# Optimization experiments

Hardware: AMD Instinct MI355X
Metric: run time of the kernel (lower is better)

The kernel has to match this reference:

```python
import jax, jax.numpy as jnp
import numpy as np

# edge types: (src_type, dst_type), order fixed to match param stack index
ETYPES = [("tag","question"),("tag","answer"),("tag","comment"),("module","question"),("module","answer"),("question","tag"),("answer","tag"),("comment","tag"),("question","module"),("answer","module")]
NTYPES = ["tag","question","answer","comment","module"]
EKEYS = ["ei_tq","ei_ta","ei_tc","ei_mq","ei_ma","ei_qt","ei_at","ei_ct","ei_qm","ei_am"]
ECOUNT = [500000,1000000,1000000,300000,600000,500000,1000000,1000000,300000,600000]
N = {"tag":5000,"question":50000,"answer":100000,"comment":150000,"module":2000}
H, D, P, G, O = 64, 256, 768, 1024, 2


def setup_inputs() -> dict:
    key = jax.random.key(0)
    ks = iter(jax.random.split(key, 80))
    inp = {}
    for t in NTYPES:
        inp["x_" + t] = jax.random.normal(next(ks), (N[t], D), jnp.float32)
    inp["post_emb"] = jax.random.normal(next(ks), (G, P), jnp.float32)
    for ek, (s, d), E in zip(EKEYS, ETYPES, ECOUNT):
        src = jax.random.randint(next(ks), (E,), 0, N[s])
        dst = jax.random.randint(next(ks), (E,), 0, N[d])
        inp[ek] = jnp.stack([src, dst])
    for t in NTYPES:
        inp["batch_" + t] = jnp.sort(jax.random.randint(next(ks), (N[t],), 0, G))
    for l, din in enumerate([D, H]):
        inp[f"Wsrc{l}"] = 0.05 * jax.random.normal(next(ks), (10, din, H), jnp.float32)
        inp[f"Wdst{l}"] = 0.05 * jax.random.normal(next(ks), (10, din, H), jnp.float32)
        inp[f"asrc{l}"] = 0.05 * jax.random.normal(next(ks), (10, H), jnp.float32)
        inp[f"adst{l}"] = 0.05 * jax.random.normal(next(ks), (10, H), jnp.float32)
        inp[f"b{l}"] = jnp.zeros((10, H), jnp.float32)
    inp["Wlin"] = 0.05 * jax.random.normal(next(ks), (5 * H + P, O), jnp.float32)
    inp["blin"] = jnp.zeros((O,), jnp.float32)
    return inp


def _gat(xs, xd, ei, Ws, Wd, a_s, a_d, b):
    # PyG GATConv (bipartite, heads=1, add_self_loops=False)
    hs = xs @ Ws                      # [Ns, H]
    hd = xd @ Wd                      # [Nd, H]
    src, dst = ei[0], ei[1]
    logits = jax.nn.leaky_relu((hs @ a_s)[src] + (hd @ a_d)[dst], 0.2)  # [E]
    nd = xd.shape[0]
    m = jax.ops.segment_max(logits, dst, num_segments=nd)
    ex = jnp.exp(logits - m[dst])
    den = jax.ops.segment_sum(ex, dst, num_segments=nd)
    alpha = ex / (den[dst] + 1e-16)
    out = jax.ops.segment_sum(hs[src] * alpha[:, None], dst, num_segments=nd)
    return out + b


def _mean_pool(x, batch, num_graphs):
    s = jax.ops.segment_sum(x, batch, num_segments=num_graphs)
    c = jax.ops.segment_sum(jnp.ones((x.shape[0],), x.dtype), batch, num_segments=num_graphs)
    return s / jnp.maximum(c, 1.0)[:, None]


def _forward(xs, eis, layers, batches, post_emb, Wlin, blin):
    x = xs
    for (Ws, Wd, a_s, a_d, b) in layers:
        new = {t: None for t in NTYPES}
        for i, (s, d) in enumerate(ETYPES):
            o = _gat(x[s], x[d], eis[i], Ws[i], Wd[i], a_s[i], a_d[i], b[i])
            new[d] = o if new[d] is None else new[d] + o
        x = {t: jax.nn.relu(v) for t, v in new.items()}
    num_graphs = post_emb.shape[0]
    pooled = [_mean_pool(x[t], batches[t], num_graphs) for t in NTYPES]
    out = jnp.concatenate(pooled + [post_emb], axis=1)   # [G, 5H + P]
    logits = jax.nn.relu(out @ Wlin + blin)
    return jax.nn.softmax(logits, axis=-1)


def reference(x_tag, x_question, x_answer, x_comment, x_module, post_emb,
              ei_tq, ei_ta, ei_tc, ei_mq, ei_ma, ei_qt, ei_at, ei_ct, ei_qm, ei_am,
              batch_tag, batch_question, batch_answer, batch_comment, batch_module,
              Wsrc0, Wdst0, asrc0, adst0, b0, Wsrc1, Wdst1, asrc1, adst1, b1,
              Wlin, blin):
    xs = {"tag": x_tag, "question": x_question, "answer": x_answer, "comment": x_comment, "module": x_module}
    eis = [ei_tq, ei_ta, ei_tc, ei_mq, ei_ma, ei_qt, ei_at, ei_ct, ei_qm, ei_am]
    batches = {"tag": batch_tag, "question": batch_question, "answer": batch_answer, "comment": batch_comment, "module": batch_module}
    layers = [(Wsrc0, Wdst0, asrc0, adst0, b0), (Wsrc1, Wdst1, asrc1, adst1, b1)]
    return _forward(xs, eis, layers, batches, post_emb, Wlin, blin)
```

## Files before the change

### kernel.cpp

```cpp
#include <hip/hip_runtime.h>
#include <math.h>

#define NTY 5
#define NET 10
#define NTOT 307000
#define ETOT 6800000
#define GDIM 1024
#define PDIM 768
#define NGEMMB 7335
#define GSH 2445
#define NBINB 1668
#define NBK 2949
#define NMEGA_C (NBINB + GSH)
#define NMEGA_B (NBINB + GSH)
#define NMEGA_S (NBK + GSH)
#define NPREPB 802

using short8 = __attribute__((ext_vector_type(8))) short;
using f32x4  = __attribute__((ext_vector_type(4))) float;

static const int kSRCT[NET]= {0,0,0,4,4,1,2,3,1,2};
static const int kNT[NTY]  = {5000,50000,100000,150000,2000};
static const int kTOFF[NTY]= {0,5000,55000,155000,305000};
static const int kRB[NET+1]= {0,50000,150000,300000,350000,450000,455000,460000,465000,467000,469000};

__device__ const int gOB[NET]   = {0,50001,150002,300003,350004,450005,455006,460007,465008,467009};
__device__ const int gEB[NET+1] = {0,500000,1500000,2500000,2800000,3400000,3900000,4900000,5900000,6200000,6800000};
__device__ const int gSB[NET]   = {0,5000,10000,15000,17000,19000,69000,169000,319000,369000};
__device__ const int gRB[NET]   = {0,50000,150000,300000,350000,450000,455000,460000,465000,467000};
__device__ const int gND[NET]   = {50000,100000,150000,50000,100000,5000,5000,5000,2000,2000};
__device__ const int gTOFF[NTY] = {0,5000,55000,155000,305000};
__device__ const int gNIN[NTY]  = {3,2,2,1,2};
__device__ const int gINET[NTY][3] = {{5,6,7},{0,3,0},{1,4,0},{2,0,0},{8,9,0}};
__device__ const int gNJ[NET]   = {3,0,0,2,0,2,2,1,0,0};
__device__ const int gTG[NET][3]= {{5,6,7},{0,0,0},{0,0,0},{8,9,0},{0,0,0},{0,3,0},{1,4,0},{2,0,0},{0,0,0},{0,0,0}};
__device__ const int gDSTT[NET] = {1,2,3,1,2,0,0,0,4,4};
__device__ const int gSH[NET]   = {8,8,8,8,8,4,4,4,4,4};
__device__ const int gBKB[NET+1]= {0,196,587,1173,1369,1760,2073,2386,2699,2824,2949};
__device__ const int gBC[NET+1] = {0,123,368,613,687,834,957,1202,1447,1521,1668};

__device__ __forceinline__ unsigned short f2bf(float f){
  unsigned int u = __float_as_uint(f);
  u += 0x7fffu + ((u>>16)&1u);
  return (unsigned short)(u>>16);
}
__device__ __forceinline__ float bf2f(unsigned short h){
  return __uint_as_float(((unsigned int)h)<<16);
}

struct PrepTab {
  const float* Wd0; const float* ad0; const float* b0;
  const float* Wd1; const float* ad1; const float* b1;
  const float* Ws0; const float* Ws1;
  float* wv0; float* wv1; float* bs0; float* bs1;
  unsigned short* Wt0; unsigned short* Wt1;
};
struct PoolTab { const int* batch[NTY]; const float* x[NTY]; int nt[NTY]; };
struct GemmArgs {
  const float* X[NET];
  const unsigned short* Wt;
  const float* asrc;
  const float* wv;
  unsigned short* hs;
  float* ssrc;
  float* sdst;
  int K;
};
struct MCTab {
  GemmArgs g;
  const int* ei[NET];
  int* cntB;
};
struct MBTab {
  GemmArgs g;
  const int* ei[NET];
  int* gcur;
  int2* pairs;
};
struct MSTab {
  GemmArgs g;
  const int2* pairs;
  const int* cntB;
  const int* segB;
  const int* exB;
  int* offs;
  int* csr;
};
struct AggTab {
  const int* offs;
  const int* csr;
  const unsigned short* hs;
  const float* ssrc;
  const float* sdst;
  const float* bsum;
  float* xout;
};

__global__ __launch_bounds__(256) void k_prep(PrepTab p) {
  int b = blockIdx.x;
  int tid = threadIdx.x;
  if (b == 0) {
    for (int e2=0; e2<NET; e2++){
      const float* W = p.Wd0 + (long)e2*256*64;
      const float* a = p.ad0 + e2*64;
      float s=0.f;
      #pragma unroll 8
      for (int c=0;c<64;c++) s += W[tid*64+c]*a[c];
      p.wv0[e2*256+tid]=s;
    }
    for (int idx=tid; idx<320; idx+=256){
      int ty=idx>>6, c=idx&63; float s=0.f;
      #pragma unroll
      for (int i=0;i<NET;i++) if (gDSTT[i]==ty) s += p.b0[i*64+c];
      p.bs0[idx]=s;
    }
    return;
  }
  if (b == 1) {
    if (tid < 64){
      for (int e2=0; e2<NET; e2++){
        const float* W = p.Wd1 + (long)e2*64*64;
        const float* a = p.ad1 + e2*64;
        float s=0.f;
        #pragma unroll 8
        for (int c=0;c<64;c++) s += W[tid*64+c]*a[c];
        p.wv1[e2*256+tid]=s;
      }
    }
    for (int idx=tid; idx<320; idx+=256){
      int ty=idx>>6, c=idx&63; float s=0.f;
      #pragma unroll
      for (int i=0;i<NET;i++) if (gDSTT[i]==ty) s += p.b1[i*64+c];
      p.bs1[idx]=s;
    }
    return;
  }
  if (b < 2+640) {
    int i = b-2;
    int et = i>>6, chunk = i&63;
    int idx = chunk*256 + tid;
    int col = idx>>8, k = idx&255;
    p.Wt0[(long)et*16384 + idx] = f2bf(p.Ws0[(long)et*16384 + k*64 + col]);
    return;
  }
  {
    int i = b-642;
    int et = i>>4, chunk = i&15;
    int idx = chunk*256 + tid;
    int col = idx>>6, k = idx&63;
    p.Wt1[(long)et*4096 + idx] = f2bf(p.Ws1[(long)et*4096 + k*64 + col]);
  }
}

__global__ __launch_bounds__(256) void k_scanB(const int* __restrict__ cntB,
                                               int* __restrict__ segB,
                                               int* __restrict__ gcurB,
                                               int* __restrict__ exB) {
  __shared__ int tp[256], te[256];
  int tid = threadIdx.x;
  int base = tid*12;
  int locP[12], locE[12];
  int sp=0, se=0;
  #pragma unroll
  for (int i=0;i<12;i++){
    int b = base+i;
    int v = (b<NBK) ? cntB[b] : 0;
    locE[i]=se; se += v;
    locP[i]=sp; sp += (v+7)&~7;
  }
  tp[tid]=sp; te[tid]=se; __syncthreads();
  for (int off=1; off<256; off<<=1){
    int xp = (tid>=off)? tp[tid-off] : 0;
    int xe = (tid>=off)? te[tid-off] : 0;
    __syncthreads();
    tp[tid]+=xp; te[tid]+=xe;
    __syncthreads();
  }
  int preP = tp[tid]-sp, preE = te[tid]-se;
  #pragma unroll
  for (int i=0;i<12;i++){
    int b = base+i;
    if (b<NBK){
      int v = preP + locP[i];
      segB[b]=v; gcurB[b]=v;
      exB[b]=preE + locE[i];
    }
  }
}

__device__ __forceinline__ void gemm_block(const GemmArgs& t, int b) {
  __shared__ unsigned short sX[64][72];
  __shared__ unsigned short sWt[64][72];
  __shared__ float sdd[3][64][4];
  const int GB1=79,GB2=158,GB3=237,GB4=269,GB5=301,GB6=1083,GB7=2646,GB8=4990,GB9=5772;
  int et = (b>=GB1)+(b>=GB2)+(b>=GB3)+(b>=GB4)+(b>=GB5)+(b>=GB6)+(b>=GB7)+(b>=GB8)+(b>=GB9);
  const int GBb[NET] = {0,GB1,GB2,GB3,GB4,GB5,GB6,GB7,GB8,GB9};
  const int NSa[NET] = {5000,5000,5000,2000,2000,50000,100000,150000,50000,100000};
  int lb = b - GBb[et];
  int Ns = NSa[et];
  int K = t.K;
  const float* X = t.X[et];
  const unsigned short* Wt = t.Wt + (long)et*64*K;
  const float* avec = t.asrc + et*64;
  int sbase = gSB[et];
  unsigned short* HS = t.hs + (long)sbase*64;
  float* score = t.ssrc + sbase;

  int nj = gNJ[et];
  const float* wvA = t.wv + gTG[et][0]*256;
  const float* wvB = t.wv + gTG[et][1]*256;
  const float* wvC = t.wv + gTG[et][2]*256;

  int tid = threadIdx.x;
  int w = tid>>6, lane = tid&63;
  int row0 = lb*64;
  int l15 = lane&15, lg = lane>>4;
  int arow = w*16 + l15;
  int kgrp = lg*8;
  int drow = tid>>2, dq = tid&3;
  f32x4 acc0={0.f,0.f,0.f,0.f}, acc1={0.f,0.f,0.f,0.f}, acc2={0.f,0.f,0.f,0.f}, acc3={0.f,0.f,0.f,0.f};
  float asd0=0.f, asd1=0.f, asd2=0.f;

  for (int k0=0;k0<K;k0+=64){
    #pragma unroll
    for (int p=0;p<4;p++){
      int r = (tid>>4) + 16*p;
      int c = (tid&15)*4;
      int gr = row0 + r;
      float4 xv = make_float4(0.f,0.f,0.f,0.f);
      if (gr < Ns) xv = *(const float4*)(X + (long)gr*K + k0 + c);
      ushort4 o; o.x=f2bf(xv.x); o.y=f2bf(xv.y); o.z=f2bf(xv.z); o.w=f2bf(xv.w);
      *(ushort4*)&sX[r][c] = o;
    }
    {
      int cq = tid>>2, kq = tid&3;
      const unsigned short* ws = Wt + (long)cq*K + k0;
      #pragma unroll
      for (int it=0; it<4; it++){
        int k = kq*4 + it*16;
        *(ushort4*)&sWt[cq][k] = *(const ushort4*)(ws + k);
      }
    }
    __syncthreads();
    #pragma unroll
    for (int ks=0; ks<64; ks+=32){
      short8 af = *(const short8*)&sX[arow][ks+kgrp];
      short8 b0 = *(const short8*)&sWt[ 0+l15][ks+kgrp];
      short8 b1 = *(const short8*)&sWt[16+l15][ks+kgrp];
      short8 b2 = *(const short8*)&sWt[32+l15][ks+kgrp];
      short8 b3 = *(const short8*)&sWt[48+l15][ks+kgrp];
      acc0 = __builtin_amdgcn_mfma_f32_16x16x32_bf16(af, b0, acc0, 0, 0, 0);
      acc1 = __builtin_amdgcn_mfma_f32_16x16x32_bf16(af, b1, acc1, 0, 0, 0);
      acc2 = __builtin_amdgcn_mfma_f32_16x16x32_bf16(af, b2, acc2, 0, 0, 0);
      acc3 = __builtin_amdgcn_mfma_f32_16x16x32_bf16(af, b3, acc3, 0, 0, 0);
    }
    if (nj) {
      int kb = dq*16;
      #pragma unroll
      for (int kk=0; kk<16; kk++){
        float xv = bf2f(sX[drow][kb+kk]);
        asd0 += xv * wvA[k0+kb+kk];
        asd1 += xv * wvB[k0+kb+kk];
        asd2 += xv * wvC[k0+kb+kk];
      }
    }
    __syncthreads();
  }
  if (nj) {
    sdd[0][drow][dq]=asd0;
    sdd[1][drow][dq]=asd1;
    sdd[2][drow][dq]=asd2;
    __syncthreads();
    if (tid < 64) {
      int r = row0 + tid;
      if (r < Ns) {
        for (int j=0;j<nj;j++) {
          float s = sdd[j][tid][0]+sdd[j][tid][1]+sdd[j][tid][2]+sdd[j][tid][3];
          t.sdst[gRB[gTG[et][j]] + r] = s;
        }
      }
    }
  }
  float av0 = avec[ 0+l15], av1 = avec[16+l15], av2 = avec[32+l15], av3 = avec[48+l15];
  int growb = row0 + w*16 + lg*4;
  #pragma unroll
  for (int r=0;r<4;r++){
    int grow = growb + r;
    if (grow < Ns){
      HS[(long)grow*64 +  0+l15] = f2bf(acc0[r]);
      HS[(long)grow*64 + 16+l15] = f2bf(acc1[r]);
      HS[(long)grow*64 + 32+l15] = f2bf(acc2[r]);
      HS[(long)grow*64 + 48+l15] = f2bf(acc3[r]);
    }
    float s = acc0[r]*av0 + acc1[r]*av1 + acc2[r]*av2 + acc3[r]*av3;
    s += __shfl_xor(s, 1);
    s += __shfl_xor(s, 2);
    s += __shfl_xor(s, 4);
    s += __shfl_xor(s, 8);
    if (l15==0 && grow<Ns) score[grow]=s;
  }
}

__global__ __launch_bounds__(256) void k_gemm_all(GemmArgs t) {
  gemm_block(t, blockIdx.x);
}

__global__ __launch_bounds__(256) void k_megaCount(MCTab t) {
  __shared__ int cnt[640];
  long long b = blockIdx.x;
  const long long G = GSH, T = NMEGA_C;
  long long lo = (b*G)/T, hi = ((b+1)*G)/T;
  if (hi > lo) {
    gemm_block(t.g, (int)lo);
    return;
  }
  int sidx = (int)(b - lo);
  int et=0;
  #pragma unroll
  for (int i=0;i<NET;i++) if (sidx >= gBC[i+1]) et=i+1;
  int lb = sidx - gBC[et];
  int E = gEB[et+1]-gEB[et];
  int e0 = lb*4096;
  int eend = e0+4096; if (eend > E) eend = E;
  int sh = gSH[et];
  int nbk = gBKB[et+1]-gBKB[et];
  const int* D = t.ei[et] + E;
  int tid = threadIdx.x;
  for (int j=tid; j<nbk; j+=256) cnt[j]=0;
  __syncthreads();
  #pragma unroll
  for (int i=0;i<16;i++){
    int idx = e0 + i*256 + tid;
    if (idx < eend) atomicAdd(&cnt[D[idx]>>sh], 1);
  }
  __syncthreads();
  int* cb = t.cntB + gBKB[et];
  for (int j=tid; j<nbk; j+=256) if (cnt[j]) atomicAdd(&cb[j], cnt[j]);
}

__global__ __launch_bounds__(256) void k_megaBin(MBTab t) {
  __shared__ int cnt[640], cnt2[640], gb2[640];
  long long b = blockIdx.x;
  const long long G = GSH, T = NMEGA_B;
  long long lo = (b*G)/T, hi = ((b+1)*G)/T;
  if (hi > lo) {
    gemm_block(t.g, GSH + (int)lo);
    return;
  }
  int sidx = (int)(b - lo);
  int et=0;
  #pragma unroll
  for (int i=0;i<NET;i++) if (sidx >= gBC[i+1]) et=i+1;
  int lb = sidx - gBC[et];
  int E = gEB[et+1]-gEB[et];
  int e0 = lb*4096;
  int eend = e0+4096; if (eend > E) eend = E;
  int sh = gSH[et];
  int nbk = gBKB[et+1]-gBKB[et];
  int bkb = gBKB[et];
  const int* EI = t.ei[et];
  int tid = threadIdx.x;
  int sr[16], dv[16];
  #pragma unroll
  for (int i=0;i<16;i++){
    int idx = e0 + i*256 + tid;
    if (idx < eend){ sr[i]=EI[idx]; dv[i]=EI[E+idx]; } else dv[i] = -1;
  }
  for (int j=tid; j<nbk; j+=256){ cnt[j]=0; cnt2[j]=0; }
  __syncthreads();
  #pragma unroll
  for (int i=0;i<16;i++) if (dv[i]>=0) atomicAdd(&cnt[dv[i]>>sh], 1);
  __syncthreads();
  for (int j=tid; j<nbk; j+=256) if (cnt[j]) gb2[j] = atomicAdd(&t.gcur[bkb+j], cnt[j]);
  __syncthreads();
  #pragma unroll
  for (int i=0;i<16;i++) if (dv[i]>=0){
    int bb = dv[i]>>sh;
    int p = gb2[bb] + atomicAdd(&cnt2[bb], 1);
    t.pairs[p] = make_int2(sr[i], dv[i]);
  }
}

__global__ __launch_bounds__(256) void k_megaScat(MSTab t) {
  __shared__ int cnt[256], sd[256], lcur[256];
  long long b = blockIdx.x;
  const long long G = GSH, T = NMEGA_S;
  long long lo = (b*G)/T, hi = ((b+1)*G)/T;
  if (hi > lo) {
    gemm_block(t.g, 2*GSH + (int)lo);
    return;
  }
  int b2 = (int)(b - lo);
  int et=0;
  #pragma unroll
  for (int i=0;i<NET;i++) if (b2 >= gBKB[i+1]) et=i+1;
  int lb = b2 - gBKB[et];
  int sh = gSH[et];
  int nd = gND[et];
  int d0 = lb<<sh;
  int ndst = (1<<sh); if (d0+ndst > nd) ndst = nd-d0;
  int n = t.cntB[b2];
  const int2* pr = t.pairs + t.segB[b2];
  int csrBase = t.exB[b2] - gEB[et];
  int tid = threadIdx.x;
  cnt[tid]=0;
  __syncthreads();
  for (int i=tid; i<n; i+=256) atomicAdd(&cnt[pr[i].y - d0], 1);
  __syncthreads();
  int v = (tid<ndst)? cnt[tid] : 0;
  sd[tid]=v; __syncthreads();
  for (int off=1; off<256; off<<=1){
    int x = (tid>=off)? sd[tid-off] : 0;
    __syncthreads();
    sd[tid]+=x;
    __syncthreads();
  }
  int excl = sd[tid]-v;
  lcur[tid] = excl;
  if (tid < ndst) t.offs[gOB[et] + d0 + tid] = csrBase + excl;
  if (tid==0 && b2 == gBKB[et+1]-1) t.offs[gOB[et] + nd] = gEB[et+1]-gEB[et];
  __syncthreads();
  int* csrb = t.csr + gEB[et] + csrBase;
  for (int i=tid; i<n; i+=256){
    int2 p = pr[i];
    int pos = atomicAdd(&lcur[p.y - d0], 1);
    csrb[pos] = p.x;
  }
}

__global__ __launch_bounds__(256) void k_agg_all(AggTab t) {
  int nb = blockIdx.x;
  int node0;
  if (nb < 1250)      node0 = nb*4;
  else if (nb < 1750) node0 = 305000 + (nb-1250)*4;
  else                node0 = 5000 + (nb-1750)*4;
  int node = node0 + (threadIdx.x>>6);
  int lane = threadIdx.x & 63;
  int ty = (node>=5000)+(node>=55000)+(node>=155000)+(node>=305000);
  int r = node - gTOFF[ty];
  float outacc = 0.f;
  int ne = gNIN[ty];
  for (int ii=0; ii<ne; ii++) {
    int et = gINET[ty][ii];
    float sd = t.sdst[gRB[et] + r];
    int ob = gOB[et];
    int beg = t.offs[ob + r];
    int end = t.offs[ob + r + 1];
    if (beg >= end) continue;
    const int* cs = t.csr + gEB[et];
    const float* ss = t.ssrc + gSB[et];
    const unsigned short* hsb = t.hs + (long)gSB[et]*64;
    float denl = 0.f, acc = 0.f;
    for (int chunk = beg; chunk < end; chunk += 64) {
      int n = end - chunk; if (n > 64) n = 64;
      int s = 0; float ex = 0.f;
      if (lane < n) {
        s = cs[chunk + lane];
        float l = ss[s] + sd;
        l = (l>0.f)? l : 0.2f*l;
        ex = __expf(l);
      }
      denl += ex;
      unsigned int exu = __float_as_uint(ex);
      int j = 0;
      for (; j+8 <= n; j += 8) {
        int a0=__builtin_amdgcn_readlane(s,j+0), a1=__builtin_amdgcn_readlane(s,j+1);
        int a2=__builtin_amdgcn_readlane(s,j+2), a3=__builtin_amdgcn_readlane(s,j+3);
        int a4=__builtin_amdgcn_readlane(s,j+4), a5=__builtin_amdgcn_readlane(s,j+5);
        int a6=__builtin_amdgcn_readlane(s,j+6), a7=__builtin_amdgcn_readlane(s,j+7);
        float e0=__uint_as_float(__builtin_amdgcn_readlane(exu,j+0));
        float e1=__uint_as_float(__builtin_amdgcn_readlane(exu,j+1));
        float e2=__uint_as_float(__builtin_amdgcn_readlane(exu,j+2));
        float e3=__uint_as_float(__builtin_amdgcn_readlane(exu,j+3));
        float e4=__uint_as_float(__builtin_amdgcn_readlane(exu,j+4));
        float e5=__uint_as_float(__builtin_amdgcn_readlane(exu,j+5));
        float e6=__uint_as_float(__builtin_amdgcn_readlane(exu,j+6));
        float e7=__uint_as_float(__builtin_amdgcn_readlane(exu,j+7));
        float h0=bf2f(hsb[(long)a0*64+lane]);
        float h1=bf2f(hsb[(long)a1*64+lane]);
        float h2=bf2f(hsb[(long)a2*64+lane]);
        float h3=bf2f(hsb[(long)a3*64+lane]);
        float h4=bf2f(hsb[(long)a4*64+lane]);
        float h5=bf2f(hsb[(long)a5*64+lane]);
        float h6=bf2f(hsb[(long)a6*64+lane]);
        float h7=bf2f(hsb[(long)a7*64+lane]);
        acc += e0*h0 + e1*h1 + e2*h2 + e3*h3;
        acc += e4*h4 + e5*h5 + e6*h6 + e7*h7;
      }
      for (; j<n; j++) {
        int aj=__builtin_amdgcn_readlane(s,j);
        float ej=__uint_as_float(__builtin_amdgcn_readlane(exu,j));
        acc += ej * bf2f(hsb[(long)aj*64+lane]);
      }
    }
    #pragma unroll
    for (int off=32; off; off>>=1) denl += __shfl_xor(denl, off);
    outacc += acc/(denl+1e-16f);
  }
  float o = outacc + t.bsum[ty*64+lane];
  t.xout[(long)node*64+lane] = fmaxf(o,0.f);
}

__global__ __launch_bounds__(64) void k_pool(PoolTab t, float* __restrict__ pooled) {
  int g = blockIdx.x; int ty = blockIdx.y; int lane = threadIdx.x;
  const int* batch = t.batch[ty];
  int n = t.nt[ty];
  int lo=0, hi=0;
  if (lane==0){
    int a=0,b2=n;
    while(a<b2){int mm=(a+b2)>>1; if (batch[mm]<g) a=mm+1; else b2=mm;}
    lo=a;
    a=lo; b2=n;
    while(a<b2){int mm=(a+b2)>>1; if (batch[mm]<g+1) a=mm+1; else b2=mm;}
    hi=a;
  }
  lo=__shfl(lo,0); hi=__shfl(hi,0);
  const float* x = t.x[ty];
  float acc=0.f;
  for (int i=lo;i<hi;i++) acc += x[(long)i*64+lane];
  int cnt = hi-lo;
  pooled[(long)g*320 + ty*64 + lane] = acc / (float)(cnt>0?cnt:1);
}

__global__ __launch_bounds__(256) void k_final(
    const float* __restrict__ pooled, const float* __restrict__ post,
    const float* __restrict__ Wlin, const float* __restrict__ blin,
    float* __restrict__ out)
{
  int w = (blockIdx.x*256+threadIdx.x)>>6;
  int lane = threadIdx.x&63;
  if (w>=GDIM) return;
  float a0=0.f,a1=0.f;
  for (int k=lane;k<320+PDIM;k+=64){
    float v = (k<320) ? pooled[(long)w*320+k] : post[(long)w*PDIM + (k-320)];
    a0 += v*Wlin[k*2];
    a1 += v*Wlin[k*2+1];
  }
  #pragma unroll
  for (int off=32;off;off>>=1){ a0+=__shfl_xor(a0,off); a1+=__shfl_xor(a1,off); }
  if (lane==0){
    float z0=a0+blin[0], z1=a1+blin[1];
    z0=fmaxf(z0,0.f); z1=fmaxf(z1,0.f);
    float mm=fmaxf(z0,z1);
    float e0=__expf(z0-mm), e1=__expf(z1-mm);
    float inv = 1.f/(e0+e1);
    out[w*2+0]=e0*inv; out[w*2+1]=e1*inv;
  }
}

extern "C" void kernel_launch(void* const* d_in, const int* in_sizes, int n_in,
                              void* d_out, int out_size, void* d_ws, size_t ws_size,
                              hipStream_t stream) {
  (void)in_sizes; (void)n_in; (void)out_size; (void)ws_size;
  char* ws = (char*)d_ws;
  size_t off = 0;
  auto A = [&](size_t nbytes){ size_t o=off; off=(off+nbytes+255)&~((size_t)255); return o; };
  size_t xbuf1_o = A((size_t)NTOT*64*4);
  size_t xbuf2_o = A((size_t)NTOT*64*4);
  size_t hs_o    = A((size_t)469000*64*2);
  size_t csr_o   = A((size_t)ETOT*4);
  size_t pairs_o = A((size_t)6832000*8);
  size_t offs_o  = A((size_t)469010*4);
  size_t ssrc_o  = A((size_t)469000*4);
  size_t sdst_o  = A((size_t)469000*4);
  size_t pool_o  = A((size_t)GDIM*320*4);
  size_t wv0_o   = A((size_t)NET*256*4);
  size_t wv1_o   = A((size_t)NET*256*4);
  size_t bs0_o   = A((size_t)320*4);
  size_t bs1_o   = A((size_t)320*4);
  size_t cntB_o  = A((size_t)NBK*4);
  size_t segB_o  = A((size_t)NBK*4);
  size_t gcurB_o = A((size_t)NBK*4);
  size_t exB_o   = A((size_t)NBK*4);
  size_t wt0_o   = A((size_t)NET*64*256*2);
  size_t wt1_o   = A((size_t)NET*64*64*2);

  float* xbuf1 = (float*)(ws + xbuf1_o);
  float* xbuf2 = (float*)(ws + xbuf2_o);
  unsigned short* hsB = (unsigned short*)(ws + hs_o);
  int*   csr   = (int*)(ws + csr_o);
  int2*  pairs = (int2*)(ws + pairs_o);
  int*   offs  = (int*)(ws + offs_o);
  float* ssrcB = (float*)(ws + ssrc_o);
  float* sdstA = (float*)(ws + sdst_o);
  float* pooled= (float*)(ws + pool_o);
  float* wv0   = (float*)(ws + wv0_o);
  float* wv1   = (float*)(ws + wv1_o);
  float* bs0   = (float*)(ws + bs0_o);
  float* bs1   = (float*)(ws + bs1_o);
  int*   cntB  = (int*)(ws + cntB_o);
  int*   segB  = (int*)(ws + segB_o);
  int*   gcurB = (int*)(ws + gcurB_o);
  int*   exB   = (int*)(ws + exB_o);
  unsigned short* Wt0 = (unsigned short*)(ws + wt0_o);
  unsigned short* Wt1 = (unsigned short*)(ws + wt1_o);

  PrepTab pp;
  pp.Wd0 = (const float*)d_in[22]; pp.ad0 = (const float*)d_in[24]; pp.b0 = (const float*)d_in[25];
  pp.Wd1 = (const float*)d_in[27]; pp.ad1 = (const float*)d_in[29]; pp.b1 = (const float*)d_in[30];
  pp.Ws0 = (const float*)d_in[21]; pp.Ws1 = (const float*)d_in[26];
  pp.wv0 = wv0; pp.wv1 = wv1; pp.bs0 = bs0; pp.bs1 = bs1;
  pp.Wt0 = Wt0; pp.Wt1 = Wt1;

  hipMemsetAsync(cntB, 0, (size_t)NBK*4, stream);
  k_prep<<<NPREPB,256,0,stream>>>(pp);

  MCTab mc;
  for (int e=0;e<NET;e++) mc.g.X[e] = (const float*)d_in[kSRCT[e]];
  mc.g.Wt = Wt0;
  mc.g.asrc = (const float*)d_in[23];
  mc.g.wv = wv0; mc.g.hs = hsB; mc.g.ssrc = ssrcB; mc.g.sdst = sdstA; mc.g.K = 256;
  for (int i=0;i<NET;i++) mc.ei[i] = (const int*)d_in[6+i];
  mc.cntB = cntB;
  k_megaCount<<<NMEGA_C,256,0,stream>>>(mc);

  k_scanB<<<1,256,0,stream>>>(cntB, segB, gcurB, exB);

  MBTab mb;
  mb.g = mc.g;
  for (int i=0;i<NET;i++) mb.ei[i] = (const int*)d_in[6+i];
  mb.gcur = gcurB; mb.pairs = pairs;
  k_megaBin<<<NMEGA_B,256,0,stream>>>(mb);

  MSTab ms;
  ms.g = mc.g;
  ms.pairs = pairs; ms.cntB = cntB; ms.segB = segB; ms.exB = exB;
  ms.offs = offs; ms.csr = csr;
  k_megaScat<<<NMEGA_S,256,0,stream>>>(ms);

  AggTab a0;
  a0.offs = offs; a0.csr = csr; a0.hs = hsB; a0.ssrc = ssrcB;
  a0.sdst = sdstA; a0.bsum = bs0; a0.xout = xbuf1;
  k_agg_all<<<NTOT/4,256,0,stream>>>(a0);

  GemmArgs g1;
  for (int e=0;e<NET;e++) g1.X[e] = (const float*)(xbuf1 + (long)kTOFF[kSRCT[e]]*64);
  g1.Wt = Wt1;
  g1.asrc = (const float*)d_in[28];
  g1.wv = wv1; g1.hs = hsB; g1.ssrc = ssrcB; g1.sdst = sdstA; g1.K = 64;
  k_gemm_all<<<NGEMMB,256,0,stream>>>(g1);

  AggTab a1;
  a1.offs = offs; a1.csr = csr; a1.hs = hsB; a1.ssrc = ssrcB;
  a1.sdst = sdstA; a1.bsum = bs1; a1.xout = xbuf2;
  k_agg_all<<<NTOT/4,256,0,stream>>>(a1);

  PoolTab pt;
  for (int t=0;t<NTY;t++){
    pt.batch[t] = (const int*)d_in[16+t];
    pt.x[t] = (const float*)(xbuf2 + (long)kTOFF[t]*64);
    pt.nt[t] = kNT[t];
  }
  dim3 pgrid(GDIM, NTY);
  k_pool<<<pgrid,64,0,stream>>>(pt, pooled);

  k_final<<<GDIM/4,256,0,stream>>>(pooled, (const float*)d_in[5],
                                   (const float*)d_in[31], (const float*)d_in[32],
                                   (float*)d_out);
}
```

Before: 1.010 ms.

## Load GEMM fragments directly from global memory, removing LDS staging and barriers

The projection GEMM block no longer stages X and W tiles through shared memory. Each lane now loads its MFMA A-fragment straight from the fp32 input row, converting to bf16 in registers, and loads its B-fragments from the transposed weights in global memory. The destination-score dot products are computed from the same registers and reduced with cross-lane shuffles instead of an LDS reduction. This drops the __syncthreads barriers and the shared-memory traffic, at the cost of redundant global loads of the weight columns across waves and less coalesced reads of X.

After: 1.034 ms. +2.4%, slower.

```diff
diff --git a/kernel.cpp b/kernel.cpp
--- a/kernel.cpp
+++ b/kernel.cpp
@@ -189,9 +189,6 @@
 }
 
 __device__ __forceinline__ void gemm_block(const GemmArgs& t, int b) {
-  __shared__ unsigned short sX[64][72];
-  __shared__ unsigned short sWt[64][72];
-  __shared__ float sdd[3][64][4];
   const int GB1=79,GB2=158,GB3=237,GB4=269,GB5=301,GB6=1083,GB7=2646,GB8=4990,GB9=5772;
   int et = (b>=GB1)+(b>=GB2)+(b>=GB3)+(b>=GB4)+(b>=GB5)+(b>=GB6)+(b>=GB7)+(b>=GB8)+(b>=GB9);
   const int GBb[NET] = {0,GB1,GB2,GB3,GB4,GB5,GB6,GB7,GB8,GB9};
@@ -215,72 +212,60 @@
   int w = tid>>6, lane = tid&63;
   int row0 = lb*64;
   int l15 = lane&15, lg = lane>>4;
-  int arow = w*16 + l15;
-  int kgrp = lg*8;
-  int drow = tid>>2, dq = tid&3;
+  int arow = row0 + w*16 + l15;
+  bool rok = arow < Ns;
+  const float* xrow = X + (long)(rok ? arow : 0)*K;
+  const unsigned short* wtc0 = Wt + (long)( 0+l15)*K;
+  const unsigned short* wtc1 = Wt + (long)(16+l15)*K;
+  const unsigned short* wtc2 = Wt + (long)(32+l15)*K;
+  const unsigned short* wtc3 = Wt + (long)(48+l15)*K;
+  int kb = lg*8;
+
   f32x4 acc0={0.f,0.f,0.f,0.f}, acc1={0.f,0.f,0.f,0.f}, acc2={0.f,0.f,0.f,0.f}, acc3={0.f,0.f,0.f,0.f};
   float asd0=0.f, asd1=0.f, asd2=0.f;
 
-  for (int k0=0;k0<K;k0+=64){
-    #pragma unroll
-    for (int p=0;p<4;p++){
-      int r = (tid>>4) + 16*p;
-      int c = (tid&15)*4;
-      int gr = row0 + r;
-      float4 xv = make_float4(0.f,0.f,0.f,0.f);
-      if (gr < Ns) xv = *(const float4*)(X + (long)gr*K + k0 + c);
-      ushort4 o; o.x=f2bf(xv.x); o.y=f2bf(xv.y); o.z=f2bf(xv.z); o.w=f2bf(xv.w);
-      *(ushort4*)&sX[r][c] = o;
-    }
-    {
-      int cq = tid>>2, kq = tid&3;
-      const unsigned short* ws = Wt + (long)cq*K + k0;
-      #pragma unroll
-      for (int it=0; it<4; it++){
-        int k = kq*4 + it*16;
-        *(ushort4*)&sWt[cq][k] = *(const ushort4*)(ws + k);
-      }
-    }
-    __syncthreads();
-    #pragma unroll
-    for (int ks=0; ks<64; ks+=32){
-      short8 af = *(const short8*)&sX[arow][ks+kgrp];
-      short8 b0 = *(const short8*)&sWt[ 0+l15][ks+kgrp];
-      short8 b1 = *(const short8*)&sWt[16+l15][ks+kgrp];
-      short8 b2 = *(const short8*)&sWt[32+l15][ks+kgrp];
-      short8 b3 = *(const short8*)&sWt[48+l15][ks+kgrp];
-      acc0 = __builtin_amdgcn_mfma_f32_16x16x32_bf16(af, b0, acc0, 0, 0, 0);
-      acc1 = __builtin_amdgcn_mfma_f32_16x16x32_bf16(af, b1, acc1, 0, 0, 0);
-      acc2 = __builtin_amdgcn_mfma_f32_16x16x32_bf16(af, b2, acc2, 0, 0, 0);
-      acc3 = __builtin_amdgcn_mfma_f32_16x16x32_bf16(af, b3, acc3, 0, 0, 0);
-    }
+  for (int k0=0; k0<K; k0+=32){
+    float4 xa = make_float4(0.f,0.f,0.f,0.f), xb = make_float4(0.f,0.f,0.f,0.f);
+    if (rok) {
+      xa = *(const float4*)(xrow + k0 + kb);
+      xb = *(const float4*)(xrow + k0 + kb + 4);
+    }
+    short8 af;
+    af[0]=(short)f2bf(xa.x); af[1]=(short)f2bf(xa.y);
+    af[2]=(short)f2bf(xa.z); af[3]=(short)f2bf(xa.w);
+    af[4]=(short)f2bf(xb.x); af[5]=(short)f2bf(xb.y);
+    af[6]=(short)f2bf(xb.z); af[7]=(short)f2bf(xb.w);
+    short8 b0 = *(const short8*)(wtc0 + k0 + kb);
+    short8 b1 = *(const short8*)(wtc1 + k0 + kb);
+    short8 b2 = *(const short8*)(wtc2 + k0 + kb);
+    short8 b3 = *(const short8*)(wtc3 + k0 + kb);
+    acc0 = __builtin_amdgcn_mfma_f32_16x16x32_bf16(af, b0, acc0, 0, 0, 0);
+    acc1 = __builtin_amdgcn_mfma_f32_16x16x32_bf16(af, b1, acc1, 0, 0, 0);
+    acc2 = __builtin_amdgcn_mfma_f32_16x16x32_bf16(af, b2, acc2, 0, 0, 0);
+    acc3 = __builtin_amdgcn_mfma_f32_16x16x32_bf16(af, b3, acc3, 0, 0, 0);
     if (nj) {
-      int kb = dq*16;
-      #pragma unroll
-      for (int kk=0; kk<16; kk++){
-        float xv = bf2f(sX[drow][kb+kk]);
-        asd0 += xv * wvA[k0+kb+kk];
-        asd1 += xv * wvB[k0+kb+kk];
-        asd2 += xv * wvC[k0+kb+kk];
-      }
-    }
-    __syncthreads();
-  }
+      asd0 += xa.x*wvA[k0+kb+0] + xa.y*wvA[k0+kb+1] + xa.z*wvA[k0+kb+2] + xa.w*wvA[k0+kb+3]
+            + xb.x*wvA[k0+kb+4] + xb.y*wvA[k0+kb+5] + xb.z*wvA[k0+kb+6] + xb.w*wvA[k0+kb+7];
+      if (nj > 1)
+        asd1 += xa.x*wvB[k0+kb+0] + xa.y*wvB[k0+kb+1] + xa.z*wvB[k0+kb+2] + xa.w*wvB[k0+kb+3]
+              + xb.x*wvB[k0+kb+4] + xb.y*wvB[k0+kb+5] + xb.z*wvB[k0+kb+6] + xb.w*wvB[k0+kb+7];
+      if (nj > 2)
+        asd2 += xa.x*wvC[k0+kb+0] + xa.y*wvC[k0+kb+1] + xa.z*wvC[k0+kb+2] + xa.w*wvC[k0+kb+3]
+              + xb.x*wvC[k0+kb+4] + xb.y*wvC[k0+kb+5] + xb.z*wvC[k0+kb+6] + xb.w*wvC[k0+kb+7];
+    }
+  }
+
   if (nj) {
-    sdd[0][drow][dq]=asd0;
-    sdd[1][drow][dq]=asd1;
-    sdd[2][drow][dq]=asd2;
-    __syncthreads();
-    if (tid < 64) {
-      int r = row0 + tid;
-      if (r < Ns) {
-        for (int j=0;j<nj;j++) {
-          float s = sdd[j][tid][0]+sdd[j][tid][1]+sdd[j][tid][2]+sdd[j][tid][3];
-          t.sdst[gRB[gTG[et][j]] + r] = s;
-        }
-      }
-    }
-  }
+    asd0 += __shfl_xor(asd0, 16); asd0 += __shfl_xor(asd0, 32);
+    asd1 += __shfl_xor(asd1, 16); asd1 += __shfl_xor(asd1, 32);
+    asd2 += __shfl_xor(asd2, 16); asd2 += __shfl_xor(asd2, 32);
+    if (lg == 0 && rok) {
+      t.sdst[gRB[gTG[et][0]] + arow] = asd0;
+      if (nj > 1) t.sdst[gRB[gTG[et][1]] + arow] = asd1;
+      if (nj > 2) t.sdst[gRB[gTG[et][2]] + arow] = asd2;
+    }
+  }
+
   float av0 = avec[ 0+l15], av1 = avec[16+l15], av2 = avec[32+l15], av3 = avec[48+l15];
   int growb = row0 + w*16 + lg*4;
   #pragma unroll
```
